# Optimization experiments

Measured on AMD Instinct MI355X. Metric: run time of the kernel, lower is better.

Reference implementation:

```python
import jax, jax.numpy as jnp
import numpy as np


def setup_inputs() -> dict:
    key = jax.random.key(0)
    k1, k2, k3, k4, k5 = jax.random.split(key, 5)
    num_chunks, input_dim, output_dim = 100000, 256, 512
    num_members, num_cells = 400000, 50000
    chunk_features = jax.random.normal(k1, (num_chunks, input_dim), dtype=jnp.float32)
    member_idx = jax.random.randint(k2, (num_members,), 0, num_chunks, dtype=jnp.int32)
    segment_ids = jnp.sort(jax.random.randint(k3, (num_members,), 0, num_cells, dtype=jnp.int32))
    W = jax.random.normal(k4, (input_dim, output_dim), dtype=jnp.float32) / np.sqrt(input_dim)
    b = jax.random.normal(k5, (output_dim,), dtype=jnp.float32) * 0.01
    return {
        "chunk_features": chunk_features,
        "member_idx": member_idx,
        "segment_ids": segment_ids,
        "num_cells": num_cells,
        "W": W,
        "b": b,
    }


def reference(chunk_features, member_idx, segment_ids, num_cells, W, b):
    # Gather per-membership chunk embeddings: (M, D)
    gathered = jnp.take(chunk_features, member_idx, axis=0)
    # Segment-sum over cells, then divide by counts -> segment mean (num_cells, D)
    sums = jax.ops.segment_sum(gathered, segment_ids, num_segments=num_cells)
    counts = jax.ops.segment_sum(
        jnp.ones((member_idx.shape[0],), dtype=chunk_features.dtype),
        segment_ids, num_segments=num_cells)
    cell_emb = sums / jnp.maximum(counts, 1.0)[:, None]
    # Linear projection (input_dim != output_dim)
    return cell_emb @ W + b
```

## Files before the change

### kernel.cpp

```cpp
#include <hip/hip_runtime.h>

typedef __attribute__((ext_vector_type(8))) short short8;
typedef __attribute__((ext_vector_type(4))) float floatx4;

static __device__ __forceinline__ unsigned short f2bf(float f) {
    unsigned int u = __float_as_uint(f);
    u = (u + 0x7FFFu + ((u >> 16) & 1u)) >> 16;
    return (unsigned short)u;
}

__global__ void starts_kernel(const int* __restrict__ seg, int M, int num_cells,
                              int* __restrict__ starts) {
    int m = blockIdx.x * blockDim.x + threadIdx.x;
    if (m > M) return;
    int prev = (m == 0) ? -1 : seg[m - 1];
    int cur  = (m == M) ? num_cells : seg[m];
    for (int c = prev + 1; c <= cur; ++c) starts[c] = m;
}

__global__ void prep_wt_kernel(const float* __restrict__ W,
                               unsigned short* __restrict__ Wt) {
    int g = blockIdx.x * blockDim.x + threadIdx.x;
    int n = g >> 8;
    int k = g & 255;
    Wt[g] = f2bf(W[k * 512 + n]);
}

__global__ void seg_mean_kernel(const float* __restrict__ chunk_features,
                                const int* __restrict__ member_idx,
                                const int* __restrict__ starts,
                                int num_cells,
                                unsigned short* __restrict__ cell_emb) {
    const int wid  = threadIdx.x >> 6;
    const int lane = threadIdx.x & 63;
    const int c = blockIdx.x * 4 + wid;

    float4 acc = make_float4(0.f, 0.f, 0.f, 0.f);
    int cnt = 0;

    if (c < num_cells) {
        const int s = starts[c];
        const int e = starts[c + 1];
        cnt = e - s;
        const float4* cf = (const float4*)chunk_features;

        for (int base = s; base < e; base += 64) {
            int m = base + lane;
            int idx = (m < e) ? member_idx[m] : 0;
            int n = e - base; if (n > 64) n = 64;
            int ci = __shfl(idx, 0);
            float4 vn = cf[(size_t)ci * 64 + lane];
            for (int j = 0; j < n - 1; ++j) {
                float4 v = vn;
                int cin = __shfl(idx, j + 1);
                vn = cf[(size_t)cin * 64 + lane];
                acc.x += v.x; acc.y += v.y; acc.z += v.z; acc.w += v.w;
            }
            acc.x += vn.x; acc.y += vn.y; acc.z += vn.z; acc.w += vn.w;
        }
    }

    float inv = 1.0f / (float)(cnt > 0 ? cnt : 1);
    ushort4 o;
    o.x = f2bf(acc.x * inv);
    o.y = f2bf(acc.y * inv);
    o.z = f2bf(acc.z * inv);
    o.w = f2bf(acc.w * inv);
    *(ushort4*)(cell_emb + (size_t)c * 256 + lane * 4) = o;
}

__global__ __launch_bounds__(256) void gemm_kernel(
        const unsigned short* __restrict__ A,
        const unsigned short* __restrict__ Bt,
        const float* __restrict__ bias,
        float* __restrict__ out,
        int Mreal) {
    constexpr int LDSS = 40;
    __shared__ unsigned short As[128 * LDSS];
    __shared__ unsigned short Bs[128 * LDSS];

    const int tid  = threadIdx.x;
    const int wid  = tid >> 6;
    const int lane = tid & 63;
    const int wm = wid & 1, wn = wid >> 1;
    const int l15 = lane & 15, q = lane >> 4;
    const int m0 = blockIdx.y * 128;
    const int n0 = blockIdx.x * 128;

    floatx4 acc[4][4] = {};

    for (int kb = 0; kb < 256; kb += 32) {
#pragma unroll
        for (int r = 0; r < 2; ++r) {
            int chunk = tid + r * 256;
            int row = chunk >> 2;
            int col = (chunk & 3) * 8;
            *(short8*)&As[row * LDSS + col] =
                *(const short8*)&A[(size_t)(m0 + row) * 256 + kb + col];
            *(short8*)&Bs[row * LDSS + col] =
                *(const short8*)&Bt[(size_t)(n0 + row) * 256 + kb + col];
        }
        __syncthreads();

        short8 af[4], bf[4];
#pragma unroll
        for (int mi = 0; mi < 4; ++mi)
            af[mi] = *(const short8*)&As[(wm * 64 + mi * 16 + l15) * LDSS + q * 8];
#pragma unroll
        for (int ni = 0; ni < 4; ++ni)
            bf[ni] = *(const short8*)&Bs[(wn * 64 + ni * 16 + l15) * LDSS + q * 8];
#pragma unroll
        for (int mi = 0; mi < 4; ++mi)
#pragma unroll
            for (int ni = 0; ni < 4; ++ni)
                acc[mi][ni] = __builtin_amdgcn_mfma_f32_16x16x32_bf16(
                    af[mi], bf[ni], acc[mi][ni], 0, 0, 0);
        __syncthreads();
    }

#pragma unroll
    for (int ni = 0; ni < 4; ++ni) {
        int n = n0 + wn * 64 + ni * 16 + l15;
        float bv = bias[n];
#pragma unroll
        for (int mi = 0; mi < 4; ++mi) {
            int mbase = m0 + wm * 64 + mi * 16 + q * 4;
#pragma unroll
            for (int r = 0; r < 4; ++r) {
                int row = mbase + r;
                if (row < Mreal)
                    out[(size_t)row * 512 + n] = acc[mi][ni][r] + bv;
            }
        }
    }
}

extern "C" void kernel_launch(void* const* d_in, const int* in_sizes, int n_in,
                              void* d_out, int out_size, void* d_ws, size_t ws_size,
                              hipStream_t stream) {
    const float* chunk_features = (const float*)d_in[0];
    const int*   member_idx     = (const int*)d_in[1];
    const int*   segment_ids    = (const int*)d_in[2];
    const float* W              = (const float*)d_in[4];
    const float* bias           = (const float*)d_in[5];
    float* out = (float*)d_out;

    const int M        = in_sizes[1];
    const int out_dim  = in_sizes[5];
    const int num_cells = out_size / out_dim;
    const int mtiles = (num_cells + 127) / 128;
    const int Mpad   = mtiles * 128;

    unsigned short* cell_emb = (unsigned short*)d_ws;
    unsigned short* Wt       = cell_emb + (size_t)Mpad * 256;
    int*            starts   = (int*)(Wt + 512 * 256);

    hipLaunchKernelGGL(starts_kernel, dim3((M + 1 + 255) / 256), dim3(256), 0, stream,
                       segment_ids, M, num_cells, starts);
    hipLaunchKernelGGL(prep_wt_kernel, dim3(512), dim3(256), 0, stream, W, Wt);
    hipLaunchKernelGGL(seg_mean_kernel, dim3(Mpad / 4), dim3(256), 0, stream,
                       chunk_features, member_idx, starts, num_cells, cell_emb);
    hipLaunchKernelGGL(gemm_kernel, dim3(4, mtiles), dim3(256), 0, stream,
                       cell_emb, Wt, bias, out, num_cells);
}
```

Measured before the change: 282.2 us.

## Balance segment-mean work across waves using LDS atomics over member ranges

```diff
diff --git a/kernel.cpp b/kernel.cpp
--- a/kernel.cpp
+++ b/kernel.cpp
@@ -26,47 +26,79 @@
     Wt[g] = f2bf(W[k * 512 + n]);
 }
 
-__global__ void seg_mean_kernel(const float* __restrict__ chunk_features,
-                                const int* __restrict__ member_idx,
-                                const int* __restrict__ starts,
-                                int num_cells,
-                                unsigned short* __restrict__ cell_emb) {
-    const int wid  = threadIdx.x >> 6;
-    const int lane = threadIdx.x & 63;
-    const int c = blockIdx.x * 4 + wid;
+#define CPB 16
+__global__ __launch_bounds__(256) void seg_mean_kernel(
+        const float* __restrict__ chunk_features,
+        const int* __restrict__ member_idx,
+        const int* __restrict__ segment_ids,
+        const int* __restrict__ starts,
+        int num_cells,
+        unsigned short* __restrict__ cell_emb) {
+    __shared__ float accs[CPB * 256];
 
-    float4 acc = make_float4(0.f, 0.f, 0.f, 0.f);
-    int cnt = 0;
+    const int tid  = threadIdx.x;
+    const int wid  = tid >> 6;
+    const int lane = tid & 63;
+    const int c0 = blockIdx.x * CPB;
 
-    if (c < num_cells) {
-        const int s = starts[c];
-        const int e = starts[c + 1];
-        cnt = e - s;
-        const float4* cf = (const float4*)chunk_features;
+#pragma unroll
+    for (int i = 0; i < CPB; ++i)
+        accs[tid + i * 256] = 0.f;
+    __syncthreads();
 
-        for (int base = s; base < e; base += 64) {
-            int m = base + lane;
-            int idx = (m < e) ? member_idx[m] : 0;
-            int n = e - base; if (n > 64) n = 64;
-            int ci = __shfl(idx, 0);
-            float4 vn = cf[(size_t)ci * 64 + lane];
-            for (int j = 0; j < n - 1; ++j) {
-                float4 v = vn;
-                int cin = __shfl(idx, j + 1);
-                vn = cf[(size_t)cin * 64 + lane];
-                acc.x += v.x; acc.y += v.y; acc.z += v.z; acc.w += v.w;
+    if (c0 < num_cells) {
+        int cend = c0 + CPB; if (cend > num_cells) cend = num_cells;
+        const int s = starts[c0];
+        const int e = starts[cend];
+
+        int m = s + wid;
+        if (m < e) {
+            int mu  = __builtin_amdgcn_readfirstlane(m);
+            int idx = member_idx[mu];
+            int cl  = segment_ids[mu] - c0;
+            while (true) {
+                int mn = m + 4;
+                bool more = mn < e;
+                int idx2 = 0, cl2 = 0;
+                if (more) {
+                    int mu2 = __builtin_amdgcn_readfirstlane(mn);
+                    idx2 = member_idx[mu2];
+                    cl2  = segment_ids[mu2] - c0;
+                }
+                const float* row = chunk_features + (size_t)idx * 256;
+                float v0 = row[lane];
+                float v1 = row[lane + 64];
+                float v2 = row[lane + 128];
+                float v3 = row[lane + 192];
+                float* a = accs + cl * 256;
+                atomicAdd(a + lane,       v0);
+                atomicAdd(a + lane + 64,  v1);
+                atomicAdd(a + lane + 128, v2);
+                atomicAdd(a + lane + 192, v3);
+                if (!more) break;
+                m = mn; idx = idx2; cl = cl2;
             }
-            acc.x += vn.x; acc.y += vn.y; acc.z += vn.z; acc.w += vn.w;
         }
     }
+    __syncthreads();
 
-    float inv = 1.0f / (float)(cnt > 0 ? cnt : 1);
-    ushort4 o;
-    o.x = f2bf(acc.x * inv);
-    o.y = f2bf(acc.y * inv);
-    o.z = f2bf(acc.z * inv);
-    o.w = f2bf(acc.w * inv);
-    *(ushort4*)(cell_emb + (size_t)c * 256 + lane * 4) = o;
+#pragma unroll
+    for (int i = 0; i < CPB / 4; ++i) {
+        int cl = wid + i * 4;
+        int c  = c0 + cl;
+        float4 v = *(float4*)(accs + cl * 256 + lane * 4);
+        float inv = 0.f;
+        if (c < num_cells) {
+            int cnt = starts[c + 1] - starts[c];
+            inv = 1.0f / (float)(cnt > 0 ? cnt : 1);
+        }
+        ushort4 o;
+        o.x = f2bf(v.x * inv);
+        o.y = f2bf(v.y * inv);
+        o.z = f2bf(v.z * inv);
+        o.w = f2bf(v.w * inv);
+        *(ushort4*)(cell_emb + (size_t)c * 256 + lane * 4) = o;
+    }
 }
 
 __global__ __launch_bounds__(256) void gemm_kernel(
@@ -158,8 +190,8 @@
     hipLaunchKernelGGL(starts_kernel, dim3((M + 1 + 255) / 256), dim3(256), 0, stream,
                        segment_ids, M, num_cells, starts);
     hipLaunchKernelGGL(prep_wt_kernel, dim3(512), dim3(256), 0, stream, W, Wt);
-    hipLaunchKernelGGL(seg_mean_kernel, dim3(Mpad / 4), dim3(256), 0, stream,
-                       chunk_features, member_idx, starts, num_cells, cell_emb);
+    hipLaunchKernelGGL(seg_mean_kernel, dim3(Mpad / CPB), dim3(256), 0, stream,
+                       chunk_features, member_idx, segment_ids, starts, num_cells, cell_emb);
     hipLaunchKernelGGL(gemm_kernel, dim3(4, mtiles), dim3(256), 0, stream,
                        cell_emb, Wt, bias, out, num_cells);
 }
```

Result: slower. 760.6 us (+169.5%).
